# Optimization experiments

Measured on AMD Instinct MI355X. Metric: run time of the kernel, lower is better.

Reference implementation:

```python
import jax, jax.numpy as jnp
import numpy as np

HIDDEN = 2048
N_HEADS = 16
N_KV_HEADS = 4
HEAD_DIM = HIDDEN // N_HEADS  # 128
FFN = 4096
N_EXPERTS = 8
TOP_K = 2
T = 2048
EPS = 1e-5
ROPE_THETA = 10000.0


def setup_inputs() -> dict:
    key = jax.random.key(0)
    ks = jax.random.split(key, 10)
    s = 0.02
    q_size = N_HEADS * HEAD_DIM
    kv_size = N_KV_HEADS * HEAD_DIM
    return {
        "hidden_states": jax.random.normal(ks[0], (T, HIDDEN), jnp.float32),
        "positions": jnp.arange(T, dtype=jnp.int32),
        "norm1_w": jnp.ones((HIDDEN,), jnp.float32),
        "norm2_w": jnp.ones((HIDDEN,), jnp.float32),
        "wqkv": jax.random.normal(ks[1], (q_size + 2 * kv_size, HIDDEN), jnp.float32) * s,
        "wo": jax.random.normal(ks[2], (HIDDEN, q_size), jnp.float32) * s,
        "gate_w": jax.random.normal(ks[3], (N_EXPERTS, HIDDEN), jnp.float32) * s,
        "w1": jax.random.normal(ks[4], (N_EXPERTS, FFN, HIDDEN), jnp.float32) * s,
        "w2": jax.random.normal(ks[5], (N_EXPERTS, HIDDEN, FFN), jnp.float32) * s,
        "w3": jax.random.normal(ks[6], (N_EXPERTS, FFN, HIDDEN), jnp.float32) * s,
    }


def _rms_norm(x, w):
    var = jnp.mean(x * x, axis=-1, keepdims=True)
    return x * jax.lax.rsqrt(var + EPS) * w


def _rope(x, positions):
    # neox-style rotary: x [T, H, D], split in halves
    half = HEAD_DIM // 2
    inv_freq = 1.0 / (ROPE_THETA ** (jnp.arange(0, half, dtype=jnp.float32) * 2.0 / HEAD_DIM))
    ang = positions.astype(jnp.float32)[:, None] * inv_freq[None, :]  # [T, half]
    cos = jnp.cos(ang)[:, None, :]  # [T, 1, half]
    sin = jnp.sin(ang)[:, None, :]
    x1, x2 = x[..., :half], x[..., half:]
    return jnp.concatenate([x1 * cos - x2 * sin, x2 * cos + x1 * sin], axis=-1)


def reference(hidden_states, positions, norm1_w, norm2_w, wqkv, wo, gate_w, w1, w2, w3):
    q_size = N_HEADS * HEAD_DIM
    kv_size = N_KV_HEADS * HEAD_DIM

    # --- input RMSNorm + attention ---
    residual = hidden_states
    h = _rms_norm(hidden_states, norm1_w)
    qkv = h @ wqkv.T  # [T, q+2kv]
    q = qkv[:, :q_size].reshape(T, N_HEADS, HEAD_DIM)
    k = qkv[:, q_size:q_size + kv_size].reshape(T, N_KV_HEADS, HEAD_DIM)
    v = qkv[:, q_size + kv_size:].reshape(T, N_KV_HEADS, HEAD_DIM)
    q = _rope(q, positions)
    k = _rope(k, positions)
    rep = N_HEADS // N_KV_HEADS
    k = jnp.repeat(k, rep, axis=1)  # [T, H, D]
    v = jnp.repeat(v, rep, axis=1)

    scale = HEAD_DIM ** -0.5
    scores = jnp.einsum('thd,shd->hts', q, k) * scale  # [H, T, T]
    causal = jnp.tril(jnp.ones((T, T), dtype=bool))
    scores = jnp.where(causal[None], scores, jnp.finfo(scores.dtype).min)
    probs = jax.nn.softmax(scores, axis=-1)
    attn = jnp.einsum('hts,shd->thd', probs, v).reshape(T, q_size)
    attn_out = attn @ wo.T

    # --- residual, post-attn RMSNorm ---
    h = attn_out + residual
    residual2 = h
    h = _rms_norm(h, norm2_w)

    # --- MoE: gate -> softmax -> top-k -> renormalize -> SwiGLU experts ---
    logits = h @ gate_w.T  # [T, E]
    routing = jax.nn.softmax(logits.astype(jnp.float32), axis=-1)
    top_vals, top_idx = jax.lax.top_k(routing, TOP_K)  # [T, K]
    top_vals = top_vals / jnp.sum(top_vals, axis=-1, keepdims=True)
    # dense per-token expert weight matrix [T, E] (zero for unselected experts)
    w_full = jnp.zeros((T, N_EXPERTS), jnp.float32).at[
        jnp.arange(T)[:, None], top_idx].add(top_vals)

    h1 = jnp.einsum('td,efd->etf', h, w1)  # [E, T, F]
    h3 = jnp.einsum('td,efd->etf', h, w3)
    g = jax.nn.silu(h1) * h3
    out_e = jnp.einsum('etf,edf->etd', g, w2)  # [E, T, D]
    moe_out = jnp.einsum('etd,te->td', out_e, w_full)

    return moe_out + residual2
```

## Files before the change

kernel.cpp:

```cpp
#include <hip/hip_runtime.h>
#include <math.h>

typedef __fp16 f16;
typedef __fp16 f16x8 __attribute__((ext_vector_type(8)));
typedef __fp16 f16x4 __attribute__((ext_vector_type(4)));
typedef float  f32x4 __attribute__((ext_vector_type(4)));

#define T_SEQ 2048
#define HID   2048
#define NQH   16
#define NKV   4
#define HD    128
#define FFN_D 4096
#define NEXP  8

#define GLDS(gp, lp) __builtin_amdgcn_global_load_lds( \
    (const __attribute__((address_space(1))) void*)(gp), \
    (__attribute__((address_space(3))) void*)(lp), 16, 0, 0)

__device__ __forceinline__ float wredsum(float v){
#pragma unroll
  for (int m = 32; m; m >>= 1) v += __shfl_xor(v, m, 64);
  return v;
}
__device__ __forceinline__ float wredmax(float v){
#pragma unroll
  for (int m = 32; m; m >>= 1) v = fmaxf(v, __shfl_xor(v, m, 64));
  return v;
}

template<bool GATHER_A, bool SCATTER_C, int EPI, int MODE>
__global__ __launch_bounds__(512, 2)
void gemm8(const f16* __restrict__ A, const f16* __restrict__ B,
           const f16* __restrict__ B2,
           void* __restrict__ Cv, void* __restrict__ Cv2,
           int K, int lda, int ldb, int ldc, long sBz,
           const int* __restrict__ grp_off, const int* __restrict__ a_rows,
           const int* __restrict__ c_rows)
{
  __shared__ __align__(16) f16 Lds[2][32768];
  const int bn = blockIdx.x, bm = blockIdx.y, z = blockIdx.z;
  int e = z, half = 0, sel = 0;
  if (MODE == 1) { e = z >> 1; half = z & 1; }
  if (MODE == 2) { e = z & 7;  sel  = z >> 3; }
  const int rowBase  = grp_off[e];
  const int rowCount = grp_off[e + 1] - rowBase;
  if (rowCount <= 0 || bm * 256 >= rowCount) return;
  const f16* Bz = ((MODE == 2 && sel) ? B2 : B) + (long)e * sBz;
  int k0 = 0, kN = K;
  if (MODE == 1) { kN = K >> 1; k0 = half * kN; }
  const int nt = kN >> 6;

  const int tid = threadIdx.x, lane = tid & 63, w = tid >> 6;
  const int wr = w >> 2, wc = w & 3;

  const int srow = w * 8 + (lane >> 3);
  const int scol = (((lane & 7) ^ (lane >> 3)) << 3);
  long aoff[4], boff[4];
#pragma unroll
  for (int i = 0; i < 4; i++) {
    int r = bm * 256 + i * 64 + srow;
    if (r > rowCount - 1) r = rowCount - 1;
    const long ar = GATHER_A ? (long)a_rows[rowBase + r] : (long)(rowBase + r);
    aoff[i] = ar * lda + scol + k0;
    boff[i] = (long)(bn * 256 + i * 64 + srow) * ldb + scol + k0;
  }

#define STG8(buf, kk) do { f16* _l = &Lds[buf][0]; \
  GLDS(A  + aoff[0] + (kk), _l +         w * 512); \
  GLDS(A  + aoff[1] + (kk), _l +  4096 + w * 512); \
  GLDS(A  + aoff[2] + (kk), _l +  8192 + w * 512); \
  GLDS(A  + aoff[3] + (kk), _l + 12288 + w * 512); \
  GLDS(Bz + boff[0] + (kk), _l + 16384 + w * 512); \
  GLDS(Bz + boff[1] + (kk), _l + 20480 + w * 512); \
  GLDS(Bz + boff[2] + (kk), _l + 24576 + w * 512); \
  GLDS(Bz + boff[3] + (kk), _l + 28672 + w * 512); } while (0)

  const int fr = lane & 15, fq = lane >> 4;
  const int cp0 = ((fq       ^ (fr & 7)) << 3);
  const int cp1 = (((4 | fq) ^ (fr & 7)) << 3);
  const int aRow = (wr * 128 + fr) * 64;
  const int bRow = 16384 + (wc * 64 + fr) * 64;

  f32x4 acc[8][4] = {};

  STG8(0, 0);
  if (nt > 1) STG8(1, 64);

  for (int kt = 0; kt < nt; kt++) {
    if (kt + 1 < nt) asm volatile("s_waitcnt vmcnt(8)" ::: "memory");
    else             asm volatile("s_waitcnt vmcnt(0)" ::: "memory");
    __builtin_amdgcn_s_barrier();
    const f16* Lb = &Lds[kt & 1][0];
    f16* Ln = &Lds[kt & 1][0];
    const bool stg = (kt + 2 < nt);
    const int kk2 = (kt + 2) * 64;
#pragma unroll
    for (int ph = 0; ph < 4; ph++) {
      const int mh = ph >> 1;
      const int cp = (ph & 1) ? cp1 : cp0;
      if (ph == 2 && stg) {
        GLDS(A + aoff[0] + kk2, Ln +        w * 512);
        GLDS(A + aoff[2] + kk2, Ln + 8192 + w * 512);
      }
      f16x8 bf[4], af[4];
#pragma unroll
      for (int n = 0; n < 4; n++)  bf[n]  = *(const f16x8*)(Lb + bRow + n * 1024 + cp);
#pragma unroll
      for (int mi = 0; mi < 4; mi++) af[mi] = *(const f16x8*)(Lb + aRow + (mh * 4 + mi) * 1024 + cp);
      __builtin_amdgcn_s_barrier();
      __builtin_amdgcn_s_setprio(1);
#pragma unroll
      for (int mi = 0; mi < 4; mi++)
#pragma unroll
        for (int n = 0; n < 4; n++)
          acc[mh * 4 + mi][n] = __builtin_amdgcn_mfma_f32_16x16x32_f16(af[mi], bf[n], acc[mh * 4 + mi][n], 0, 0, 0);
      __builtin_amdgcn_s_setprio(0);
      __builtin_amdgcn_s_barrier();
    }
    if (stg) {
      GLDS(A  + aoff[1] + kk2, Ln +  4096 + w * 512);
      GLDS(A  + aoff[3] + kk2, Ln + 12288 + w * 512);
      GLDS(Bz + boff[0] + kk2, Ln + 16384 + w * 512);
      GLDS(Bz + boff[1] + kk2, Ln + 20480 + w * 512);
      GLDS(Bz + boff[2] + kk2, Ln + 24576 + w * 512);
      GLDS(Bz + boff[3] + kk2, Ln + 28672 + w * 512);
    }
  }
#undef STG8

  float* Cf = (MODE == 1 && half) ? (float*)Cv2 : (float*)Cv;
  f16*   Ch = (MODE == 2 && sel)  ? (f16*)Cv2   : (f16*)Cv;
  const int ccol0 = bn * 256 + wc * 64 + fr;
#pragma unroll
  for (int m = 0; m < 8; m++) {
#pragma unroll
    for (int r = 0; r < 4; r++) {
      const int g = bm * 256 + wr * 128 + m * 16 + fq * 4 + r;
      if (g >= rowCount) continue;
      const long orow = SCATTER_C ? (long)c_rows[rowBase + g] : (long)(rowBase + g);
#pragma unroll
      for (int n = 0; n < 4; n++) {
        const long idx = orow * ldc + (ccol0 + n * 16);
        if (EPI == 3) Ch[idx] = (f16)acc[m][n][r];
        else          Cf[idx] = acc[m][n][r];
      }
    }
  }
}

template<int EPI, int CAUSAL, bool PVK>
__global__ __launch_bounds__(512, 2)
void gemm83(const f16* __restrict__ Ah, const f16* __restrict__ Al,
            const f16* __restrict__ Bh, const f16* __restrict__ Bl,
            void* __restrict__ Cv, int K, int lda, int ldb, int ldc,
            long sAz, long sBz, int bdiv, long sCz,
            const float* __restrict__ resid)
{
  __shared__ __align__(16) f16 Lds[2][32768];
  const int bn = blockIdx.x, bm = blockIdx.y, z = blockIdx.z;
  if (CAUSAL == 1 && bn > bm) return;
  int head = z, chunk = 0;
  if (PVK) { head = z & 7; chunk = z >> 3; }
  int kstart = 0, kend = K;
  if (PVK) {
    const int km = (bm + 1) * 128;
    if (km < kend) kend = km;
    kstart = chunk * 1024;
    if (kstart >= kend) return;
    if (kend > kstart + 1024) kend = kstart + 1024;
  }
  const int nt = (kend - kstart) >> 6;

  const f16* Ahz = Ah + (long)head * sAz;
  const f16* Alz = Al + (long)head * sAz;
  const long zb = (long)(bdiv ? head / bdiv : head) * sBz;
  const f16* Bhz = Bh + zb;
  const f16* Blz = Bl + zb;

  const int tid = threadIdx.x, lane = tid & 63, w = tid >> 6;
  const int wr = w >> 2, wc = w & 3;

  const int srow = w * 8 + (lane >> 3);
  const int scol = (((lane & 7) ^ (lane >> 3)) << 3);
  long ar[2], br[2];
#pragma unroll
  for (int i = 0; i < 2; i++) {
    ar[i] = (long)(bm * 128 + i * 64 + srow) * lda + scol + kstart;
    br[i] = (long)(bn * 128 + i * 64 + srow) * ldb + scol + kstart;
  }

#define STG83(buf, kk) do { f16* _l = &Lds[buf][0]; \
  GLDS(Ahz + ar[0] + (kk), _l +         w * 512); GLDS(Ahz + ar[1] + (kk), _l +  4096 + w * 512); \
  GLDS(Alz + ar[0] + (kk), _l +  8192 + w * 512); GLDS(Alz + ar[1] + (kk), _l + 12288 + w * 512); \
  GLDS(Bhz + br[0] + (kk), _l + 16384 + w * 512); GLDS(Bhz + br[1] + (kk), _l + 20480 + w * 512); \
  GLDS(Blz + br[0] + (kk), _l + 24576 + w * 512); GLDS(Blz + br[1] + (kk), _l + 28672 + w * 512); } while (0)

  const int fr = lane & 15, fq = lane >> 4;
  const int cp0 = ((fq       ^ (fr & 7)) << 3);
  const int cp1 = (((4 | fq) ^ (fr & 7)) << 3);
  const int aRow = (wr * 64 + fr) * 64;
  const int bRow = 16384 + (wc * 32 + fr) * 64;

  f32x4 acc[4][2] = {};

  STG83(0, 0);
  if (nt > 1) STG83(1, 64);

  for (int kt = 0; kt < nt; kt++) {
    if (kt + 1 < nt) asm volatile("s_waitcnt vmcnt(8)" ::: "memory");
    else             asm volatile("s_waitcnt vmcnt(0)" ::: "memory");
    __builtin_amdgcn_s_barrier();
    const f16* Lb = &Lds[kt & 1][0];
#pragma unroll
    for (int ks = 0; ks < 2; ks++) {
      const int cp = ks ? cp1 : cp0;
      f16x8 ah[4], al[4], bh[2], bl[2];
#pragma unroll
      for (int n = 0; n < 2; n++) {
        bh[n] = *(const f16x8*)(Lb + bRow +        n * 1024 + cp);
        bl[n] = *(const f16x8*)(Lb + bRow + 8192 + n * 1024 + cp);
      }
#pragma unroll
      for (int m = 0; m < 4; m++) {
        ah[m] = *(const f16x8*)(Lb + aRow +        m * 1024 + cp);
        al[m] = *(const f16x8*)(Lb + aRow + 8192 + m * 1024 + cp);
      }
      __builtin_amdgcn_s_setprio(1);
#pragma unroll
      for (int m = 0; m < 4; m++)
#pragma unroll
        for (int n = 0; n < 2; n++) {
          acc[m][n] = __builtin_amdgcn_mfma_f32_16x16x32_f16(ah[m], bh[n], acc[m][n], 0, 0, 0);
          acc[m][n] = __builtin_amdgcn_mfma_f32_16x16x32_f16(ah[m], bl[n], acc[m][n], 0, 0, 0);
          acc[m][n] = __builtin_amdgcn_mfma_f32_16x16x32_f16(al[m], bh[n], acc[m][n], 0, 0, 0);
        }
      __builtin_amdgcn_s_setprio(0);
    }
    __builtin_amdgcn_s_barrier();
    if (kt + 2 < nt) STG83(kt & 1, (kt + 2) * 64);
  }
#undef STG83

  float* Cf = (float*)Cv + (long)head * sCz + (PVK ? (long)chunk * T_SEQ * HID : 0);
  const int crow0 = bm * 128 + wr * 64 + fq * 4;
  const int ccol0 = bn * 128 + wc * 32 + fr;
#pragma unroll
  for (int m = 0; m < 4; m++) {
#pragma unroll
    for (int r = 0; r < 4; r++) {
      const long row = crow0 + m * 16 + r;
#pragma unroll
      for (int n = 0; n < 2; n++) {
        const long idx = row * ldc + (ccol0 + n * 16);
        const float v = acc[m][n][r];
        if (EPI == 2) Cf[idx] = v + resid[idx];
        else          Cf[idx] = v;
      }
    }
  }
}

template<bool SPLIT>
__global__ __launch_bounds__(256)
void rmsnorm_k(const float* __restrict__ x, const float* __restrict__ w,
               f16* __restrict__ hi, f16* __restrict__ lo, float* __restrict__ invr_out)
{
  const int t = blockIdx.x, tid = threadIdx.x;
  const float4* xr = (const float4*)(x + (long)t * HID);
  const float4 a = xr[tid * 2], b = xr[tid * 2 + 1];
  float ss = a.x*a.x + a.y*a.y + a.z*a.z + a.w*a.w
           + b.x*b.x + b.y*b.y + b.z*b.z + b.w*b.w;
  ss = wredsum(ss);
  __shared__ float red[4];
  if ((tid & 63) == 0) red[tid >> 6] = ss;
  __syncthreads();
  const float tot  = red[0] + red[1] + red[2] + red[3];
  const float invr = 1.0f / sqrtf(tot * (1.0f / HID) + 1e-5f);
  if (invr_out && tid == 0) invr_out[t] = invr;
  const float4* wr4 = (const float4*)w;
  const float4 wa = wr4[tid * 2], wb = wr4[tid * 2 + 1];
  const float vals[8] = { a.x*wa.x, a.y*wa.y, a.z*wa.z, a.w*wa.w,
                          b.x*wb.x, b.y*wb.y, b.z*wb.z, b.w*wb.w };
  f16x8 hv, lv;
#pragma unroll
  for (int j = 0; j < 8; j++) {
    const float y = vals[j] * invr;
    const f16 h = (f16)y;
    hv[j] = h;
    if (SPLIT) lv[j] = (f16)(y - (float)h);
  }
  const long base = (long)t * HID + tid * 8;
  *(f16x8*)(hi + base) = hv;
  if (SPLIT) *(f16x8*)(lo + base) = lv;
}

__global__ __launch_bounds__(256)
void rope_split_k(const float* __restrict__ qkv, const int* __restrict__ pos,
                  f16* __restrict__ qh, f16* __restrict__ ql,
                  f16* __restrict__ kh, f16* __restrict__ kl,
                  f16* __restrict__ vh, f16* __restrict__ vl)
{
  const int t = blockIdx.x, tid = threadIdx.x;
  __shared__ float invf[64];
  if (tid < 64) {
    const float y = (float)tid * (1.0f / 64.0f);
    invf[tid] = 1.0f / (float)pow(10000.0, (double)y);
  }
  __syncthreads();
  const float p = (float)pos[t];
  const float* row = qkv + (long)t * 3072;

#pragma unroll
  for (int i = 0; i < 4; i++) {
    const int pi = tid + i * 256;
    const int h = pi >> 6, d = pi & 63;
    const float ang = p * invf[d];
    float s, c; sincosf(ang, &s, &c);
    const float x1 = row[h * 128 + d], x2 = row[h * 128 + 64 + d];
    const float o1 = x1 * c - x2 * s;
    const float o2 = x2 * c + x1 * s;
    const long base = ((long)h * T_SEQ + t) * HD;
    { const f16 hh = (f16)o1; qh[base + d]      = hh; ql[base + d]      = (f16)(o1 - (float)hh); }
    { const f16 hh = (f16)o2; qh[base + 64 + d] = hh; ql[base + 64 + d] = (f16)(o2 - (float)hh); }
  }
  {
    const int g = tid >> 6, d = tid & 63;
    const float ang = p * invf[d];
    float s, c; sincosf(ang, &s, &c);
    const float x1 = row[2048 + g * 128 + d], x2 = row[2048 + g * 128 + 64 + d];
    const float o1 = x1 * c - x2 * s;
    const float o2 = x2 * c + x1 * s;
    const long base = ((long)g * T_SEQ + t) * HD;
    { const f16 hh = (f16)o1; kh[base + d]      = hh; kl[base + d]      = (f16)(o1 - (float)hh); }
    { const f16 hh = (f16)o2; kh[base + 64 + d] = hh; kl[base + 64 + d] = (f16)(o2 - (float)hh); }
  }
#pragma unroll
  for (int i = 0; i < 2; i++) {
    const int e = tid + i * 256;
    const int g = e >> 7, d = e & 127;
    const float v = row[2560 + e];
    const long idx = ((long)g * HD + d) * T_SEQ + t;
    const f16 h = (f16)v; vh[idx] = h; vl[idx] = (f16)(v - (float)h);
  }
}

__global__ __launch_bounds__(256)
void softmax_pack(float* __restrict__ S)
{
  const int row  = blockIdx.x * 4 + (threadIdx.x >> 6);
  const int lane = threadIdx.x & 63;
  const int t    = row & (T_SEQ - 1);
  const int nseg = (t >> 8) + 1;
  float* Sr = S + (long)row * T_SEQ;
  float4 v[8];
  const float4* Sr4 = (const float4*)Sr;
#pragma unroll
  for (int i = 0; i < 8; i++) if (i < nseg) v[i] = Sr4[i * 64 + lane];
  const float scale = 0.08838834764831843f;
  float vmax = -3.4e38f;
#pragma unroll
  for (int i = 0; i < 8; i++) {
    if (i >= nseg) continue;
    float* pv = (float*)&v[i];
    const int s0 = (i * 64 + lane) * 4;
#pragma unroll
    for (int j = 0; j < 4; j++) {
      const float xx = (s0 + j <= t) ? pv[j] * scale : -3.4e38f;
      pv[j] = xx;
      vmax = fmaxf(vmax, xx);
    }
  }
  vmax = wredmax(vmax);
  float sum = 0.f;
#pragma unroll
  for (int i = 0; i < 8; i++) {
    if (i >= nseg) continue;
    float* pv = (float*)&v[i];
#pragma unroll
    for (int j = 0; j < 4; j++) {
      const float e = (pv[j] > -3.0e38f) ? __expf(pv[j] - vmax) : 0.f;
      pv[j] = e; sum += e;
    }
  }
  sum = wredsum(sum);
  const float rinv = 1.0f / sum;
  __syncthreads();
  f16* P = (f16*)Sr;
#pragma unroll
  for (int i = 0; i < 8; i++) {
    if (i >= nseg) continue;
    const int s0 = (i * 64 + lane) * 4;
    float* pv = (float*)&v[i];
    f16x4 hv, lv;
#pragma unroll
    for (int j = 0; j < 4; j++) {
      const float pr = pv[j] * rinv;
      const f16 ph = (f16)pr;
      hv[j] = ph; lv[j] = (f16)(pr - (float)ph);
    }
    *(f16x4*)(P + s0)         = hv;
    *(f16x4*)(P + T_SEQ + s0) = lv;
  }
}

__global__ __launch_bounds__(256)
void gate_topk(const float* __restrict__ h2, const float* __restrict__ invr,
               const float* __restrict__ n2w, const float* __restrict__ gw,
               int* __restrict__ top_idx, float* __restrict__ top_w)
{
  const int t = blockIdx.x, tid = threadIdx.x;
  const float r = invr[t];
  const float4* xr = (const float4*)(h2 + (long)t * HID);
  const float4 a = xr[tid * 2], b = xr[tid * 2 + 1];
  const float4* wr4 = (const float4*)n2w;
  const float4 wa = wr4[tid * 2], wb = wr4[tid * 2 + 1];
  const float hn[8] = { a.x*wa.x*r, a.y*wa.y*r, a.z*wa.z*r, a.w*wa.w*r,
                        b.x*wb.x*r, b.y*wb.y*r, b.z*wb.z*r, b.w*wb.w*r };
  float part[8];
#pragma unroll
  for (int e = 0; e < 8; e++) {
    const float4* g4 = (const float4*)(gw + (long)e * HID + tid * 8);
    const float4 ga = g4[0], gb = g4[1];
    part[e] = hn[0]*ga.x + hn[1]*ga.y + hn[2]*ga.z + hn[3]*ga.w
            + hn[4]*gb.x + hn[5]*gb.y + hn[6]*gb.z + hn[7]*gb.w;
  }
#pragma unroll
  for (int e = 0; e < 8; e++) part[e] = wredsum(part[e]);
  __shared__ float red[4][8];
  if ((tid & 63) == 0) {
#pragma unroll
    for (int e = 0; e < 8; e++) red[tid >> 6][e] = part[e];
  }
  __syncthreads();
  if (tid == 0) {
    float lg[8];
#pragma unroll
    for (int e = 0; e < 8; e++) lg[e] = red[0][e] + red[1][e] + red[2][e] + red[3][e];
    int i1 = 0;
    for (int e = 1; e < 8; e++) if (lg[e] > lg[i1]) i1 = e;
    int i2 = -1;
    for (int e = 0; e < 8; e++) { if (e == i1) continue; if (i2 < 0 || lg[e] > lg[i2]) i2 = e; }
    const float q = expf(lg[i2] - lg[i1]);
    top_idx[t * 2] = i1; top_idx[t * 2 + 1] = i2;
    top_w[t * 2]     = 1.0f / (1.0f + q);
    top_w[t * 2 + 1] = q / (1.0f + q);
  }
}

__global__ __launch_bounds__(256)
void route_build(const int* __restrict__ ti, int* __restrict__ goff,
                 int* __restrict__ arows, int* __restrict__ crows)
{
  __shared__ int cnt[8], cur[8], off[9];
  const int tid = threadIdx.x;
  if (tid < 8) { cnt[tid] = 0; cur[tid] = 0; }
  __syncthreads();
  for (int i = tid; i < 2 * T_SEQ; i += 256) atomicAdd(&cnt[ti[i]], 1);
  __syncthreads();
  if (tid == 0) {
    int s = 0;
    for (int e = 0; e < NEXP; e++) { off[e] = s; s += cnt[e]; }
    off[NEXP] = s;
    for (int e = 0; e <= NEXP; e++) goff[e] = off[e];
  }
  __syncthreads();
  for (int i = tid; i < 2 * T_SEQ; i += 256) {
    const int e = ti[i];
    const int p = atomicAdd(&cur[e], 1);
    const int slot = off[e] + p;
    arows[slot] = i >> 1;
    crows[slot] = (i & 1) * T_SEQ + (i >> 1);
  }
}

__global__ __launch_bounds__(256)
void silu_mul_k(const f16* __restrict__ h1, const f16* __restrict__ h3, f16* __restrict__ g)
{
  const long i = ((long)blockIdx.x * 256 + threadIdx.x) * 8;
  const f16x8 a = *(const f16x8*)(h1 + i);
  const f16x8 b = *(const f16x8*)(h3 + i);
  f16x8 o;
#pragma unroll
  for (int j = 0; j < 8; j++) {
    const float xx = (float)a[j];
    const float s = xx / (1.0f + __expf(-xx));
    o[j] = (f16)(s * (float)b[j]);
  }
  *(f16x8*)(g + i) = o;
}

__global__ __launch_bounds__(256)
void split_pair_k(const float* __restrict__ src, f16* __restrict__ hi, f16* __restrict__ lo)
{
  const long i = ((long)blockIdx.x * 256 + threadIdx.x) * 8;
  const float4 a = *(const float4*)(src + i);
  const float4 b = *(const float4*)(src + i + 4);
  const float vals[8] = {a.x,a.y,a.z,a.w,b.x,b.y,b.z,b.w};
  f16x8 hv, lv;
#pragma unroll
  for (int j = 0; j < 8; j++) { const f16 h = (f16)vals[j]; hv[j] = h; lv[j] = (f16)(vals[j] - (float)h); }
  *(f16x8*)(hi + i) = hv;
  *(f16x8*)(lo + i) = lv;
}

__global__ __launch_bounds__(256)
void split_sum_k(const float* __restrict__ c0, const float* __restrict__ c1,
                 f16* __restrict__ hi, f16* __restrict__ lo)
{
  const long i = ((long)blockIdx.x * 256 + threadIdx.x) * 8;
  const int t = (int)(i >> 11);
  const float4 a = *(const float4*)(c0 + i);
  const float4 b = *(const float4*)(c0 + i + 4);
  float4 ca = {0,0,0,0}, cb = {0,0,0,0};
  if (t >= 1024) { ca = *(const float4*)(c1 + i); cb = *(const float4*)(c1 + i + 4); }
  const float vals[8] = {a.x+ca.x, a.y+ca.y, a.z+ca.z, a.w+ca.w,
                         b.x+cb.x, b.y+cb.y, b.z+cb.z, b.w+cb.w};
  f16x8 hv, lv;
#pragma unroll
  for (int j = 0; j < 8; j++) { const f16 h = (f16)vals[j]; hv[j] = h; lv[j] = (f16)(vals[j] - (float)h); }
  *(f16x8*)(hi + i) = hv;
  *(f16x8*)(lo + i) = lv;
}

__global__ __launch_bounds__(256)
void conv_f16_k(const float* __restrict__ src, f16* __restrict__ dst)
{
  const long i = ((long)blockIdx.x * 256 + threadIdx.x) * 8;
  const float4 a = *(const float4*)(src + i);
  const float4 b = *(const float4*)(src + i + 4);
  f16x8 o;
  o[0]=(f16)a.x; o[1]=(f16)a.y; o[2]=(f16)a.z; o[3]=(f16)a.w;
  o[4]=(f16)b.x; o[5]=(f16)b.y; o[6]=(f16)b.z; o[7]=(f16)b.w;
  *(f16x8*)(dst + i) = o;
}

__global__ __launch_bounds__(256)
void combine_k(const float* __restrict__ h2, const float* __restrict__ c0,
               const float* __restrict__ c1, const float* __restrict__ tw,
               float* __restrict__ out)
{
  const long i = ((long)blockIdx.x * 256 + threadIdx.x) * 4;
  const int t = (int)(i >> 11);
  const float w0 = tw[t * 2], w1 = tw[t * 2 + 1];
  const float4 a   = *(const float4*)(h2 + i);
  const float4 p0a = *(const float4*)(c0 + i);
  const float4 p0b = *(const float4*)(c1 + i);
  const float4 p1a = *(const float4*)(c0 + (long)T_SEQ * HID + i);
  const float4 p1b = *(const float4*)(c1 + (long)T_SEQ * HID + i);
  float4 o;
  o.x = a.x + w0 * (p0a.x + p0b.x) + w1 * (p1a.x + p1b.x);
  o.y = a.y + w0 * (p0a.y + p0b.y) + w1 * (p1a.y + p1b.y);
  o.z = a.z + w0 * (p0a.z + p0b.z) + w1 * (p1a.z + p1b.z);
  o.w = a.w + w0 * (p0a.w + p0b.w) + w1 * (p1a.w + p1b.w);
  *(float4*)(out + i) = o;
}

extern "C" void kernel_launch(void* const* d_in, const int* in_sizes, int n_in,
                              void* d_out, int out_size, void* d_ws, size_t ws_size,
                              hipStream_t stream)
{
  const float* x    = (const float*)d_in[0];
  const int*   pos  = (const int*)d_in[1];
  const float* n1w  = (const float*)d_in[2];
  const float* n2w  = (const float*)d_in[3];
  const float* wqkv = (const float*)d_in[4];
  const float* wo   = (const float*)d_in[5];
  const float* gw   = (const float*)d_in[6];
  const float* w1   = (const float*)d_in[7];
  const float* w2   = (const float*)d_in[8];
  const float* w3   = (const float*)d_in[9];
  float* out = (float*)d_out;

  char* base = (char*)d_ws;
  size_t off = 0;
  auto alloc = [&](size_t bytes) -> char* {
    char* r = base + off;
    off += (bytes + 255) & ~(size_t)255;
    return r;
  };
  f16* w1h = (f16*)alloc((size_t)NEXP * FFN_D * HID * 2);
  f16* w3h = (f16*)alloc((size_t)NEXP * FFN_D * HID * 2);
  f16* w2h = (f16*)alloc((size_t)NEXP * FFN_D * HID * 2);
  f16* wqh = (f16*)alloc((size_t)3072 * HID * 2);
  f16* wql = (f16*)alloc((size_t)3072 * HID * 2);
  f16* woh = (f16*)alloc((size_t)HID * HID * 2);
  f16* wol = (f16*)alloc((size_t)HID * HID * 2);
  f16* qh  = (f16*)alloc((size_t)NQH * T_SEQ * HD * 2);
  f16* ql  = (f16*)alloc((size_t)NQH * T_SEQ * HD * 2);
  f16* kh  = (f16*)alloc((size_t)NKV * T_SEQ * HD * 2);
  f16* kl  = (f16*)alloc((size_t)NKV * T_SEQ * HD * 2);
  f16* vh  = (f16*)alloc((size_t)NKV * T_SEQ * HD * 2);
  f16* vl  = (f16*)alloc((size_t)NKV * T_SEQ * HD * 2);
  float* h2      = (float*)alloc((size_t)T_SEQ * HID * 4);
  f16*   h2n     = (f16*)alloc((size_t)T_SEQ * HID * 2);
  float* contrib = (float*)alloc((size_t)2 * T_SEQ * HID * 4);
  float* invr2 = (float*)alloc(T_SEQ * 4);
  int*   tidx  = (int*)alloc(T_SEQ * 2 * 4);
  float* twt   = (float*)alloc(T_SEQ * 2 * 4);
  int*   counts = (int*)alloc(256);
  int*   goff   = (int*)alloc(256);
  int*   arows  = (int*)alloc(2 * T_SEQ * 4);
  int*   crows  = (int*)alloc(2 * T_SEQ * 4);
  (void)counts;
  char* uA = alloc((size_t)T_SEQ * 3072 * 4);
  float* qkvf = (float*)uA;
  char* uB = alloc((size_t)T_SEQ * HID * 2);
  f16* hh = (f16*)uB; f16* ahh = (f16*)uB;
  char* uC = alloc((size_t)T_SEQ * HID * 2);
  f16* hl = (f16*)uC; f16* ahl = (f16*)uC;
  char* uS = alloc((size_t)8 * T_SEQ * T_SEQ * 4);
  float* Sbuf = (float*)uS;
  f16* h1b = (f16*)uS;
  f16* h3b = (f16*)(uS + (size_t)2 * T_SEQ * FFN_D * 2);
  f16* gb  = (f16*)(uS + (size_t)4 * T_SEQ * FFN_D * 2);
  float* contribH = (float*)(uS + (size_t)6 * T_SEQ * FFN_D * 2);

  if (off > ws_size) return;

  conv_f16_k<<<(NEXP * FFN_D * HID) / (256 * 8), 256, 0, stream>>>(w1, w1h);
  conv_f16_k<<<(NEXP * FFN_D * HID) / (256 * 8), 256, 0, stream>>>(w3, w3h);
  conv_f16_k<<<(NEXP * FFN_D * HID) / (256 * 8), 256, 0, stream>>>(w2, w2h);
  split_pair_k<<<(3072 * HID) / (256 * 8), 256, 0, stream>>>(wqkv, wqh, wql);
  split_pair_k<<<(HID * HID) / (256 * 8), 256, 0, stream>>>(wo, woh, wol);

  rmsnorm_k<true><<<T_SEQ, 256, 0, stream>>>(x, n1w, hh, hl, nullptr);
  gemm83<0,0,false><<<dim3(3072/128, T_SEQ/128, 1), 512, 0, stream>>>(
      hh, hl, wqh, wql, qkvf, HID, HID, HID, 3072, 0, 0, 0, 0, nullptr);
  rope_split_k<<<T_SEQ, 256, 0, stream>>>(qkvf, pos, qh, ql, kh, kl, vh, vl);

  for (int grp = 0; grp < 2; grp++) {
    const f16* qh_g = qh + (size_t)grp * 8 * T_SEQ * HD;
    const f16* ql_g = ql + (size_t)grp * 8 * T_SEQ * HD;
    const f16* kh_g = kh + (size_t)grp * 2 * T_SEQ * HD;
    const f16* kl_g = kl + (size_t)grp * 2 * T_SEQ * HD;
    const f16* vh_g = vh + (size_t)grp * 2 * HD * T_SEQ;
    const f16* vl_g = vl + (size_t)grp * 2 * HD * T_SEQ;
    float* attn_g = contrib + (size_t)grp * 8 * HD;
    gemm83<0,1,false><<<dim3(T_SEQ/128, T_SEQ/128, 8), 512, 0, stream>>>(
        qh_g, ql_g, kh_g, kl_g, Sbuf, HD, HD, HD, T_SEQ,
        (long)T_SEQ * HD, (long)T_SEQ * HD, 4, (long)T_SEQ * T_SEQ, nullptr);
    softmax_pack<<<8 * T_SEQ / 4, 256, 0, stream>>>(Sbuf);
    gemm83<0,0,true><<<dim3(1, T_SEQ/128, 16), 512, 0, stream>>>(
        (const f16*)Sbuf, (const f16*)Sbuf + T_SEQ, vh_g, vl_g, attn_g,
        T_SEQ, 2 * T_SEQ, T_SEQ, HID,
        (long)T_SEQ * 2 * T_SEQ, (long)HD * T_SEQ, 4, HD, nullptr);
  }

  split_sum_k<<<(T_SEQ * HID) / (256 * 8), 256, 0, stream>>>(contrib, contrib + (size_t)T_SEQ * HID, ahh, ahl);
  gemm83<2,0,false><<<dim3(HID/128, T_SEQ/128, 1), 512, 0, stream>>>(
      ahh, ahl, woh, wol, h2, HID, HID, HID, HID, 0, 0, 0, 0, x);

  rmsnorm_k<false><<<T_SEQ, 256, 0, stream>>>(h2, n2w, h2n, nullptr, invr2);
  gate_topk<<<T_SEQ, 256, 0, stream>>>(h2, invr2, n2w, gw, tidx, twt);
  route_build<<<1, 256, 0, stream>>>(tidx, goff, arows, crows);

  gemm8<true,false,3,2><<<dim3(FFN_D/256, 8, 2 * NEXP), 512, 0, stream>>>(
      h2n, w1h, w3h, h1b, h3b, HID, HID, HID, FFN_D, (long)FFN_D * HID, goff, arows, nullptr);
  silu_mul_k<<<(2 * T_SEQ * FFN_D) / (256 * 8), 256, 0, stream>>>(h1b, h3b, gb);
  gemm8<false,true,0,1><<<dim3(HID/256, 8, 2 * NEXP), 512, 0, stream>>>(
      gb, w2h, nullptr, contrib, contribH, FFN_D, FFN_D, FFN_D, HID, (long)HID * FFN_D, goff, nullptr, crows);
  combine_k<<<(T_SEQ * HID) / (256 * 4), 256, 0, stream>>>(h2, contrib, contribH, twt, out);
}
```

Before: 990.8 us.

## Shrink MoE grouped GEMM tiles to 128x128 with 256 threads and K=32 stages

The MoE expert GEMM kernel moves from 256x256 tiles with 512 threads and 64-wide K stages to 128x128 tiles with 256 threads and 32-wide K stages. The pipeline is simplified to a single LDS read phase followed by an early prefetch issue, and offsets are now 32-bit. Smaller tiles waste less work on partially filled expert row groups and allow more resident blocks. In exchange, each loaded element is reused less, so global and LDS traffic per FLOP rise and barriers occur more often.

```diff
diff --git a/kernel.cpp b/kernel.cpp
--- a/kernel.cpp
+++ b/kernel.cpp
@@ -30,7 +30,7 @@
 }
 
 template<bool GATHER_A, bool SCATTER_C, int EPI, int MODE>
-__global__ __launch_bounds__(512, 2)
+__global__ __launch_bounds__(256, 4)
 void gemm8(const f16* __restrict__ A, const f16* __restrict__ B,
            const f16* __restrict__ B2,
            void* __restrict__ Cv, void* __restrict__ Cv2,
@@ -38,105 +38,82 @@
            const int* __restrict__ grp_off, const int* __restrict__ a_rows,
            const int* __restrict__ c_rows)
 {
-  __shared__ __align__(16) f16 Lds[2][32768];
+  __shared__ __align__(16) f16 Lds[2][8192];
   const int bn = blockIdx.x, bm = blockIdx.y, z = blockIdx.z;
   int e = z, half = 0, sel = 0;
   if (MODE == 1) { e = z >> 1; half = z & 1; }
   if (MODE == 2) { e = z & 7;  sel  = z >> 3; }
   const int rowBase  = grp_off[e];
   const int rowCount = grp_off[e + 1] - rowBase;
-  if (rowCount <= 0 || bm * 256 >= rowCount) return;
+  if (rowCount <= 0 || bm * 128 >= rowCount) return;
   const f16* Bz = ((MODE == 2 && sel) ? B2 : B) + (long)e * sBz;
   int k0 = 0, kN = K;
   if (MODE == 1) { kN = K >> 1; k0 = half * kN; }
-  const int nt = kN >> 6;
+  const int nt = kN >> 5;
 
   const int tid = threadIdx.x, lane = tid & 63, w = tid >> 6;
-  const int wr = w >> 2, wc = w & 3;
-
-  const int srow = w * 8 + (lane >> 3);
-  const int scol = (((lane & 7) ^ (lane >> 3)) << 3);
-  long aoff[4], boff[4];
-#pragma unroll
-  for (int i = 0; i < 4; i++) {
-    int r = bm * 256 + i * 64 + srow;
+  const int wr = w >> 1, wc = w & 1;
+
+  const int srow = tid >> 2;
+  const int scol = (((tid & 3) ^ ((tid >> 3) & 3)) << 3);
+  int aoff[2], boff[2];
+#pragma unroll
+  for (int i = 0; i < 2; i++) {
+    int r = bm * 128 + i * 64 + srow;
     if (r > rowCount - 1) r = rowCount - 1;
-    const long ar = GATHER_A ? (long)a_rows[rowBase + r] : (long)(rowBase + r);
+    const int ar = GATHER_A ? a_rows[rowBase + r] : (rowBase + r);
     aoff[i] = ar * lda + scol + k0;
-    boff[i] = (long)(bn * 256 + i * 64 + srow) * ldb + scol + k0;
+    boff[i] = (bn * 128 + i * 64 + srow) * ldb + scol + k0;
   }
 
 #define STG8(buf, kk) do { f16* _l = &Lds[buf][0]; \
-  GLDS(A  + aoff[0] + (kk), _l +         w * 512); \
-  GLDS(A  + aoff[1] + (kk), _l +  4096 + w * 512); \
-  GLDS(A  + aoff[2] + (kk), _l +  8192 + w * 512); \
-  GLDS(A  + aoff[3] + (kk), _l + 12288 + w * 512); \
-  GLDS(Bz + boff[0] + (kk), _l + 16384 + w * 512); \
-  GLDS(Bz + boff[1] + (kk), _l + 20480 + w * 512); \
-  GLDS(Bz + boff[2] + (kk), _l + 24576 + w * 512); \
-  GLDS(Bz + boff[3] + (kk), _l + 28672 + w * 512); } while (0)
+  GLDS(A  + aoff[0] + (kk), _l +        w * 512); \
+  GLDS(A  + aoff[1] + (kk), _l + 2048 + w * 512); \
+  GLDS(Bz + boff[0] + (kk), _l + 4096 + w * 512); \
+  GLDS(Bz + boff[1] + (kk), _l + 6144 + w * 512); } while (0)
 
   const int fr = lane & 15, fq = lane >> 4;
-  const int cp0 = ((fq       ^ (fr & 7)) << 3);
-  const int cp1 = (((4 | fq) ^ (fr & 7)) << 3);
-  const int aRow = (wr * 128 + fr) * 64;
-  const int bRow = 16384 + (wc * 64 + fr) * 64;
-
-  f32x4 acc[8][4] = {};
+  const int cp = ((fq ^ ((fr >> 1) & 3)) << 3);
+  const int aRow = (wr * 64 + fr) * 32;
+  const int bRow = 4096 + (wc * 64 + fr) * 32;
+
+  f32x4 acc[4][4] = {};
 
   STG8(0, 0);
-  if (nt > 1) STG8(1, 64);
+  if (nt > 1) STG8(1, 32);
 
   for (int kt = 0; kt < nt; kt++) {
-    if (kt + 1 < nt) asm volatile("s_waitcnt vmcnt(8)" ::: "memory");
+    if (kt + 1 < nt) asm volatile("s_waitcnt vmcnt(4)" ::: "memory");
     else             asm volatile("s_waitcnt vmcnt(0)" ::: "memory");
     __builtin_amdgcn_s_barrier();
     const f16* Lb = &Lds[kt & 1][0];
-    f16* Ln = &Lds[kt & 1][0];
-    const bool stg = (kt + 2 < nt);
-    const int kk2 = (kt + 2) * 64;
-#pragma unroll
-    for (int ph = 0; ph < 4; ph++) {
-      const int mh = ph >> 1;
-      const int cp = (ph & 1) ? cp1 : cp0;
-      if (ph == 2 && stg) {
-        GLDS(A + aoff[0] + kk2, Ln +        w * 512);
-        GLDS(A + aoff[2] + kk2, Ln + 8192 + w * 512);
-      }
-      f16x8 bf[4], af[4];
-#pragma unroll
-      for (int n = 0; n < 4; n++)  bf[n]  = *(const f16x8*)(Lb + bRow + n * 1024 + cp);
-#pragma unroll
-      for (int mi = 0; mi < 4; mi++) af[mi] = *(const f16x8*)(Lb + aRow + (mh * 4 + mi) * 1024 + cp);
-      __builtin_amdgcn_s_barrier();
-      __builtin_amdgcn_s_setprio(1);
-#pragma unroll
-      for (int mi = 0; mi < 4; mi++)
-#pragma unroll
-        for (int n = 0; n < 4; n++)
-          acc[mh * 4 + mi][n] = __builtin_amdgcn_mfma_f32_16x16x32_f16(af[mi], bf[n], acc[mh * 4 + mi][n], 0, 0, 0);
-      __builtin_amdgcn_s_setprio(0);
-      __builtin_amdgcn_s_barrier();
-    }
-    if (stg) {
-      GLDS(A  + aoff[1] + kk2, Ln +  4096 + w * 512);
-      GLDS(A  + aoff[3] + kk2, Ln + 12288 + w * 512);
-      GLDS(Bz + boff[0] + kk2, Ln + 16384 + w * 512);
-      GLDS(Bz + boff[1] + kk2, Ln + 20480 + w * 512);
-      GLDS(Bz + boff[2] + kk2, Ln + 24576 + w * 512);
-      GLDS(Bz + boff[3] + kk2, Ln + 28672 + w * 512);
-    }
+    f16x8 bf[4], af[4];
+#pragma unroll
+    for (int n = 0; n < 4; n++) bf[n] = *(const f16x8*)(Lb + bRow + n * 512 + cp);
+#pragma unroll
+    for (int m = 0; m < 4; m++) af[m] = *(const f16x8*)(Lb + aRow + m * 512 + cp);
+    asm volatile("s_waitcnt lgkmcnt(0)" ::: "memory");
+    __builtin_amdgcn_sched_barrier(0);
+    __builtin_amdgcn_s_barrier();
+    if (kt + 2 < nt) STG8(kt & 1, (kt + 2) * 32);
+    __builtin_amdgcn_s_setprio(1);
+#pragma unroll
+    for (int m = 0; m < 4; m++)
+#pragma unroll
+      for (int n = 0; n < 4; n++)
+        acc[m][n] = __builtin_amdgcn_mfma_f32_16x16x32_f16(af[m], bf[n], acc[m][n], 0, 0, 0);
+    __builtin_amdgcn_s_setprio(0);
   }
 #undef STG8
 
   float* Cf = (MODE == 1 && half) ? (float*)Cv2 : (float*)Cv;
   f16*   Ch = (MODE == 2 && sel)  ? (f16*)Cv2   : (f16*)Cv;
-  const int ccol0 = bn * 256 + wc * 64 + fr;
-#pragma unroll
-  for (int m = 0; m < 8; m++) {
+  const int ccol0 = bn * 128 + wc * 64 + fr;
+#pragma unroll
+  for (int m = 0; m < 4; m++) {
 #pragma unroll
     for (int r = 0; r < 4; r++) {
-      const int g = bm * 256 + wr * 128 + m * 16 + fq * 4 + r;
+      const int g = bm * 128 + wr * 64 + m * 16 + fq * 4 + r;
       if (g >= rowCount) continue;
       const long orow = SCATTER_C ? (long)c_rows[rowBase + g] : (long)(rowBase + g);
 #pragma unroll
@@ -655,10 +632,10 @@
   gate_topk<<<T_SEQ, 256, 0, stream>>>(h2, invr2, n2w, gw, tidx, twt);
   route_build<<<1, 256, 0, stream>>>(tidx, goff, arows, crows);
 
-  gemm8<true,false,3,2><<<dim3(FFN_D/256, 8, 2 * NEXP), 512, 0, stream>>>(
+  gemm8<true,false,3,2><<<dim3(FFN_D/128, 16, 2 * NEXP), 256, 0, stream>>>(
       h2n, w1h, w3h, h1b, h3b, HID, HID, HID, FFN_D, (long)FFN_D * HID, goff, arows, nullptr);
   silu_mul_k<<<(2 * T_SEQ * FFN_D) / (256 * 8), 256, 0, stream>>>(h1b, h3b, gb);
-  gemm8<false,true,0,1><<<dim3(HID/256, 8, 2 * NEXP), 512, 0, stream>>>(
+  gemm8<false,true,0,1><<<dim3(HID/128, 16, 2 * NEXP), 256, 0, stream>>>(
       gb, w2h, nullptr, contrib, contribH, FFN_D, FFN_D, FFN_D, HID, (long)HID * FFN_D, goff, nullptr, crows);
   combine_k<<<(T_SEQ * HID) / (256 * 4), 256, 0, stream>>>(h2, contrib, contribH, twt, out);
 }
```

After: 998.3 us. Within noise of the previous version (+0.8%).
